# Performance work log

Measured on AMD Instinct MI355X. Metric: run time of the kernel, lower is better.

## Reference

```python
import math
import jax, jax.numpy as jnp
import numpy as np

B, T, E, H = 8, 2048, 512, 8
NQ_H, NL = 4, 2          # qubits per attention head, circuit layers
NQ_F, FFN = 8, 2048      # FFN qubits, ffn_dim

# ---- batched state-vector quantum simulation -------------------------------
# state shape: [N, 2, 2, ..., 2] (one axis of size 2 per qubit; wire q = axis q+1)

def apply_ry(state, q, theta):
    """RY(theta) on wire q. theta: scalar or [N] (per-batch angle)."""
    th = jnp.asarray(theta) * 0.5
    c, s = jnp.cos(th), jnp.sin(th)
    if th.ndim == 1:
        shp = (-1,) + (1,) * (state.ndim - 2)
        c, s = c.reshape(shp), s.reshape(shp)
    s0 = jax.lax.index_in_dim(state, 0, axis=q + 1, keepdims=False)
    s1 = jax.lax.index_in_dim(state, 1, axis=q + 1, keepdims=False)
    return jnp.stack([c * s0 - s * s1, s * s0 + c * s1], axis=q + 1)

def apply_cnot(state, ctrl, tgt):
    c0 = jax.lax.index_in_dim(state, 0, axis=ctrl + 1, keepdims=True)
    c1 = jax.lax.index_in_dim(state, 1, axis=ctrl + 1, keepdims=True)
    c1 = jnp.flip(c1, axis=tgt + 1)  # X on target when control = 1
    return jnp.concatenate([c0, c1], axis=ctrl + 1)

def run_circuit(x, params):
    """x: [N, n] data angles. params: [L, n] (shared) or [N, L, n] (per-element).
    Circuit: L x (RY(params) layer + CNOT chain + ring CNOT), then RY(x), then <Z_q>.
    Returns [N, n] PauliZ expectations."""
    N, n = x.shape
    L = params.shape[-2]
    state = jnp.zeros((N, 2 ** n), x.dtype).at[:, 0].set(1.0).reshape((N,) + (2,) * n)
    for l in range(L):
        for q in range(n):
            theta = params[:, l, q] if params.ndim == 3 else params[l, q]
            state = apply_ry(state, q, theta)
        for q in range(n - 1):
            state = apply_cnot(state, q, q + 1)
        state = apply_cnot(state, n - 1, 0)
    for q in range(n):
        state = apply_ry(state, q, x[:, q])
    probs = (state ** 2).reshape(N, 2 ** n)
    bits = (jnp.arange(2 ** n)[:, None] >> (n - 1 - jnp.arange(n))) & 1  # wire 0 = MSB
    return probs @ (1 - 2 * bits).astype(x.dtype)  # [N, n]

def layer_norm(x, g, b, eps=1e-5):
    m = x.mean(-1, keepdims=True)
    v = ((x - m) ** 2).mean(-1, keepdims=True)
    return (x - m) / jnp.sqrt(v + eps) * g + b

def setup_inputs() -> dict:
    key = jax.random.key(0)
    ks = jax.random.split(key, 9)
    def lin(k, o, i):
        return jax.random.normal(k, (o, i), jnp.float32) / np.sqrt(i).astype(np.float32)
    return {
        "x": jax.random.normal(ks[0], (B, T, E), jnp.float32),
        "wq": lin(ks[1], E, E), "wk": lin(ks[2], E, E),
        "wv": lin(ks[3], E, E), "wo": lin(ks[4], E, E),
        "head_params": jax.random.normal(ks[5], (H, NL, NQ_H), jnp.float32),
        "ffn_params": jax.random.normal(ks[6], (2, NQ_F), jnp.float32),
        "w1": lin(ks[7], FFN, NQ_F), "w2": lin(ks[8], E, FFN),
        "g1": jnp.ones((E,), jnp.float32), "b1": jnp.zeros((E,), jnp.float32),
        "g2": jnp.ones((E,), jnp.float32), "b2": jnp.zeros((E,), jnp.float32),
    }

def reference(x, wq, wk, wv, wo, head_params, ffn_params, w1, w2, g1, b1, g2, b2):
    Bb, Tt, Ee = x.shape
    hd = Ee // H
    BT = Bb * Tt
    # ---- quantum multi-head attention (dropout = eval/identity) ----
    q = x @ wq.T; k = x @ wk.T; v = x @ wv.T
    scores = jnp.einsum('bte,bse->bts', q, k) / math.sqrt(Ee)  # NOTE: scale by sqrt(E)
    attn = jax.nn.softmax(scores, axis=-1)
    out = jnp.einsum('bts,bse->bte', attn, v)                  # [B,T,E]
    oh = out.reshape(Bb, Tt, H, hd)
    # fold heads into the batch dim; per-head params broadcast per element
    xh = oh[..., :NQ_H].transpose(2, 0, 1, 3).reshape(H * BT, NQ_H)
    ph = jnp.broadcast_to(head_params[:, None], (H, BT, NL, NQ_H)).reshape(H * BT, NL, NQ_H)
    qout = run_circuit(xh, ph)                                  # [H*BT, NQ_H]
    qout = jnp.pad(qout, ((0, 0), (0, hd - NQ_H)))              # zero-pad to head_dim
    qout = qout.reshape(H, Bb, Tt, hd).transpose(1, 2, 0, 3).reshape(Bb, Tt, Ee)
    attn_out = qout @ wo.T
    x1 = layer_norm(x + attn_out, g1, b1)
    # ---- quantum FFN (only ffn_params[0] used, as in source) ----
    xf = x1.reshape(BT, Ee)[:, :NQ_F]
    f = run_circuit(xf, ffn_params[:1]).reshape(Bb, Tt, NQ_F)
    f = jax.nn.relu(f @ w1.T) @ w2.T
    return layer_norm(x1 + f, g2, b2)
```

## Files before the change

kernel.cpp:

```cpp
#include <hip/hip_runtime.h>
#include <hip/hip_bf16.h>
#include <math.h>


#define B_   8
#define T_   2048
#define E_   512

typedef __attribute__((ext_vector_type(8))) short bf16x8;
typedef __attribute__((ext_vector_type(4))) short bf16x4;
typedef __attribute__((ext_vector_type(4))) float f32x4;

#define GLL16(g, l) __builtin_amdgcn_global_load_lds((const __attribute__((address_space(1))) void*)(g), (__attribute__((address_space(3))) void*)(l), 16, 0, 0)

__device__ inline unsigned short f2bf(float f){
  union { float f; unsigned u; } v; v.f = f;
  unsigned r = v.u + 0x7fff + ((v.u >> 16) & 1);
  return (unsigned short)(r >> 16);
}

__global__ __launch_bounds__(256) void k0_setup(const float* __restrict__ hp,
                         const float* __restrict__ fp,
                         const float* __restrict__ wo, float* __restrict__ cAB,
                         unsigned short* __restrict__ wo32b) {
  int t = threadIdx.x, bi = blockIdx.x;
  if (bi > 0) {
    int gid = (bi-1)*256 + t;
    int e = gid >> 3, c4 = gid & 7;
    float4 v = *(const float4*)(wo + (size_t)e*512 + c4*64);
    unsigned short h[4] = { f2bf(v.x), f2bf(v.y), f2bf(v.z), f2bf(v.w) };
    *(unsigned long long*)(wo32b + (size_t)e*32 + c4*4) = *(unsigned long long*)h;
    return;
  }
  __shared__ float fst[256], tmp[256], ra[256], rb[256];
  fst[t] = (t == 0) ? 1.f : 0.f;
  __syncthreads();
  #pragma unroll
  for (int q = 0; q < 8; ++q) {
    int str = 1 << (7-q);
    float th = 0.5f * fp[q];
    float c = cosf(th), s = sinf(th);
    float self = fst[t], part = fst[t ^ str];
    float nv = (t & str) ? (c*self + s*part) : (c*self - s*part);
    __syncthreads();
    tmp[t] = nv;
    __syncthreads();
    fst[t] = tmp[t];
    __syncthreads();
  }
  #pragma unroll
  for (int g = 0; g < 8; ++g) {
    int ctrl = (g < 7) ? g : 7, tgt = (g < 7) ? g+1 : 0;
    int cs = 1 << (7-ctrl), tsr = 1 << (7-tgt);
    float nv = fst[(t & cs) ? (t ^ tsr) : t];
    __syncthreads();
    fst[t] = nv;
    __syncthreads();
  }
  #pragma unroll
  for (int q = 0; q < 8; ++q) {
    int str = 1 << (7-q);
    float a = fst[t]*fst[t] * ((t & str) ? -1.f : 1.f);
    float b = fst[t]*fst[t ^ str];
    ra[t] = a; rb[t] = b;
    __syncthreads();
    for (int off = 128; off > 0; off >>= 1){
      if (t < off){ ra[t] += ra[t+off]; rb[t] += rb[t+off]; }
      __syncthreads();
    }
    if (t == 0){ cAB[64+q] = ra[0]; cAB[72+q] = rb[0]; }
    __syncthreads();
  }
  if (t < 8) {
    float st[16];
    #pragma unroll
    for (int i=0;i<16;i++) st[i]=0.f;
    st[0]=1.f;
    for (int l=0;l<2;l++){
      for (int q=0;q<4;q++){
        float th = 0.5f*hp[t*8 + l*4 + q];
        float c = cosf(th), s = sinf(th);
        int str = 1<<(3-q);
        for (int i=0;i<16;i++) if (!(i & str)) {
          float s0=st[i], s1=st[i|str];
          st[i]     = c*s0 - s*s1;
          st[i|str] = s*s0 + c*s1;
        }
      }
      for (int q=0;q<4;q++){
        int ctrl = (q<3)? q : 3, tgt = (q<3)? q+1 : 0;
        int cs = 1<<(3-ctrl), tsr = 1<<(3-tgt);
        for (int i=0;i<16;i++) if ((i&cs) && !(i&tsr)) {
          float tt = st[i]; st[i]=st[i|tsr]; st[i|tsr]=tt;
        }
      }
    }
    for (int q=0;q<4;q++){
      int str = 1<<(3-q);
      float A=0.f, Bv=0.f;
      for (int i=0;i<16;i++){
        A  += st[i]*st[i] * ((i&str)? -1.f : 1.f);
        Bv += st[i]*st[i^str];
      }
      cAB[t*4+q]    = A;
      cAB[32+t*4+q] = Bv;
    }
  }
}

__global__ __launch_bounds__(256) void kc_cast(const float* __restrict__ x,
                     const float* __restrict__ wq, const float* __restrict__ wk,
                     const float* __restrict__ w2, const float* __restrict__ wv,
                     unsigned short* __restrict__ xb, unsigned short* __restrict__ wqkb,
                     unsigned short* __restrict__ w2b, unsigned short* __restrict__ wv32b){
  int bi = blockIdx.x;
  if (bi < 4096) {
    int i = bi*256 + threadIdx.x;
    const float4* p = (const float4*)x + (size_t)i*2;
    float4 a = p[0], b = p[1];
    union { unsigned short h[8]; uint4 u; } o;
    o.h[0]=f2bf(a.x); o.h[1]=f2bf(a.y); o.h[2]=f2bf(a.z); o.h[3]=f2bf(a.w);
    o.h[4]=f2bf(b.x); o.h[5]=f2bf(b.y); o.h[6]=f2bf(b.z); o.h[7]=f2bf(b.w);
    ((uint4*)xb)[i] = o.u;
    return;
  }
  int i = (bi-4096)*256 + threadIdx.x;
  const float* src; unsigned short* dst; float s = 1.f;
  if (i < 65536){
    int row = i >> 6, c8 = (i & 63)*8;
    if (row < 512){ src = wq + (size_t)row*512 + c8; s = 0.044194173824159216f; }
    else          { src = wk + (size_t)(row-512)*512 + c8; }
    dst = wqkb + (size_t)row*512 + c8;
  } else if (i < 196608){
    int j = i - 65536;
    src = w2 + (size_t)j*8; dst = w2b + (size_t)j*8;
  } else {
    int j = i - 196608;
    int r = j >> 6, c8 = (j & 63)*8;
    src = wv + (size_t)((r>>2)*64 + (r&3))*512 + c8;
    dst = wv32b + (size_t)r*512 + c8;
  }
  float4 a = *(const float4*)src, b = *(const float4*)(src+4);
  union { unsigned short h[8]; uint4 u; } o;
  o.h[0]=f2bf(a.x*s); o.h[1]=f2bf(a.y*s); o.h[2]=f2bf(a.z*s); o.h[3]=f2bf(a.w*s);
  o.h[4]=f2bf(b.x*s); o.h[5]=f2bf(b.y*s); o.h[6]=f2bf(b.z*s); o.h[7]=f2bf(b.w*s);
  *(uint4*)dst = o.u;
}

template<int K, int LDC, bool OUTBF, int GX, int GM>
__global__ __launch_bounds__(256,2) void gemm_bt(
    const unsigned short* __restrict__ A, const unsigned short* __restrict__ Bw,
    void* __restrict__ C, int m_base){
  __shared__ __align__(16) char sm[16384];
  char* As = sm; char* Bs = sm + 8192;
  int t = threadIdx.x, w = t>>6, l = t&63;
  int lr = l&15, quad = l>>4;
  int lin = blockIdx.x;
  int n0 = ((lin >> 3) % GX) * 128;
  int m0 = ((lin & 7) * (GM/8) + lin / (8*GX)) * 128;
  int wr = (w>>1)*64, wc = (w&1)*64;
  f32x4 acc[4][4] = {};
  for (int k0 = 0; k0 < K; k0 += 32){
    __syncthreads();
    #pragma unroll
    for (int c = 0; c < 2; ++c){
      int ch = c*256 + t, row = ch>>2, sw = ch&3, lc = sw ^ ((row>>1)&3);
      GLL16(A  + (size_t)(m0+row)*K + k0 + lc*8, As + c*4096 + w*1024);
      GLL16(Bw + (size_t)(n0+row)*K + k0 + lc*8, Bs + c*4096 + w*1024);
    }
    __syncthreads();
    bf16x8 af[4], bg[4];
    #pragma unroll
    for (int i=0;i<4;++i){
      int ra = wr + i*16 + lr;
      af[i] = *(const bf16x8*)(As + ra*64 + (quad ^ ((ra>>1)&3))*16);
      int rb = wc + i*16 + lr;
      bg[i] = *(const bf16x8*)(Bs + rb*64 + (quad ^ ((rb>>1)&3))*16);
    }
    #pragma unroll
    for (int i=0;i<4;++i)
      #pragma unroll
      for (int j=0;j<4;++j)
        acc[i][j] = __builtin_amdgcn_mfma_f32_16x16x32_bf16(af[i], bg[j], acc[i][j], 0,0,0);
  }
  #pragma unroll
  for (int i=0;i<4;++i)
    #pragma unroll
    for (int j=0;j<4;++j)
      #pragma unroll
      for (int r=0;r<4;++r){
        size_t row = (size_t)(m_base + m0 + wr + i*16 + quad*4 + r);
        int col = n0 + wc + j*16 + lr;
        if constexpr (OUTBF) ((unsigned short*)C)[row*LDC + col] = f2bf(acc[i][j][r]);
        else                 ((float*)C)[row*LDC + col] = acc[i][j][r];
      }
}

__global__ __launch_bounds__(256) void k1_v32m(const unsigned short* __restrict__ xb,
    const unsigned short* __restrict__ wv32b, unsigned short* __restrict__ v32t){
  __shared__ __align__(16) char sm1[98304];
  char* Xs = sm1; char* Ws = sm1 + 65536;
  int t = threadIdx.x, w = t>>6, l = t&63, lr = l&15, quad = l>>4;
  int m0 = blockIdx.x * 64;
  #pragma unroll
  for (int i=0;i<16;++i){
    int p = i*256 + t, ks = p>>8, c2 = p&255, row = c2>>2, swp = c2&3;
    int lc = swp ^ ((row>>1)&3);
    GLL16(xb + (size_t)(m0+row)*512 + ks*32 + lc*8, Xs + (p>>6)*1024);
  }
  #pragma unroll
  for (int i=0;i<8;++i){
    int p = i*256 + t, ks = p>>7, c2 = p&127, row = c2>>2, swp = c2&3;
    int lc = swp ^ ((row>>1)&3);
    GLL16(wv32b + (size_t)row*512 + ks*32 + lc*8, Ws + (p>>6)*1024);
  }
  __syncthreads();
  f32x4 acc[2] = {};
  #pragma unroll
  for (int ks=0; ks<16; ++ks){
    int xrow = w*16 + lr;
    bf16x8 bq = *(const bf16x8*)(Xs + ks*4096 + xrow*64 + (quad ^ ((xrow>>1)&3))*16);
    #pragma unroll
    for (int ni=0; ni<2; ++ni){
      int wrow = ni*16 + lr;
      bf16x8 af = *(const bf16x8*)(Ws + ks*2048 + wrow*64 + (quad ^ ((wrow>>1)&3))*16);
      acc[ni] = __builtin_amdgcn_mfma_f32_16x16x32_bf16(af, bq, acc[ni], 0,0,0);
    }
  }
  int bb = m0 >> 11, sbase = (m0 & 2047) + w*16 + lr;
  #pragma unroll
  for (int ni=0; ni<2; ++ni)
    #pragma unroll
    for (int r=0; r<4; ++r){
      int c = ni*16 + quad*4 + r;
      v32t[((size_t)(bb*32 + c))*2048 + sbase] = f2bf(acc[ni][r]);
    }
}

__global__ __launch_bounds__(256,2) void k2_attn(
    const unsigned short* __restrict__ qkb, const unsigned short* __restrict__ v32t,
    float* __restrict__ Opart, float* __restrict__ mlb){
  __shared__ __align__(16) char sm[77824];
  char* Qc  = sm;
  char* Ks  = sm + 16384;
  char* Vts = sm + 49152;
  float* OtL = (float*)sm;
  float* mL  = (float*)(sm + 73728);
  float* lL  = (float*)(sm + 75776);

  int t = threadIdx.x, w = t>>6, l = t&63;
  int lr = l & 15, quad = l >> 4;
  int lin = blockIdx.x;
  int b = lin & 7;
  int m0 = ((lin >> 3) & 15) * 128;
  int half = lin >> 7;
  size_t bT = (size_t)b*2048;
  const char* qbase = (const char*)qkb + (bT + m0)*2048;
  const char* vbase = (const char*)v32t + (size_t)b*32*4096;

  f32x4 Ot[2][8] = {};
  float mold[8], lsum[8];
  #pragma unroll
  for (int qj=0;qj<8;++qj){ mold[qj] = -1e30f; lsum[qj] = 0.f; }

  for (int st = 0; st < 2; ++st){
    int s0 = (half*2 + st)*256;
    const char* kbase = (const char*)qkb + (bT + s0)*2048 + 1024;
    __syncthreads();
    {
      int j = t>>3, seg = t&7;
      const uint4* vs = (const uint4*)(vbase + (size_t)j*4096 + (s0 + seg*32)*2);
      uint4* vd = (uint4*)(Vts + j*528 + seg*64);
      vd[0]=vs[0]; vd[1]=vs[1]; vd[2]=vs[2]; vd[3]=vs[3];
    }
    f32x4 acc[4][8] = {};
    for (int ec = 0; ec < 8; ++ec){
      __syncthreads();
      #pragma unroll
      for (int u = 0; u < 4; ++u){
        int kk = u>>1, c = u&1;
        int ch = c*256 + t, row = ch>>2, sw = ch&3, lc = sw ^ ((row>>1)&3);
        GLL16(qbase + (size_t)row*2048 + ec*128 + kk*64 + lc*16,
              Qc + kk*8192 + c*4096 + w*1024);
      }
      #pragma unroll
      for (int rd = 0; rd < 4; ++rd){
        int ch = rd*256 + t, row = ch>>2, sw = ch&3, lc = sw ^ ((row>>1)&3);
        GLL16(kbase + (size_t)row*2048 + ec*128 +      lc*16, Ks +         rd*4096 + w*1024);
        GLL16(kbase + (size_t)row*2048 + ec*128 + 64 + lc*16, Ks + 16384 + rd*4096 + w*1024);
      }
      __syncthreads();
      #pragma unroll
      for (int kk = 0; kk < 2; ++kk){
        bf16x8 af[4];
        #pragma unroll
        for (int si = 0; si < 4; ++si){
          int row = w*64 + si*16 + lr;
          af[si] = *(const bf16x8*)(Ks + kk*16384 + row*64 + (quad ^ ((row>>1)&3))*16);
        }
        #pragma unroll
        for (int qh = 0; qh < 2; ++qh){
          bf16x8 bq[4];
          #pragma unroll
          for (int jj = 0; jj < 4; ++jj){
            int row = (qh*4+jj)*16 + lr;
            bq[jj] = *(const bf16x8*)(Qc + kk*8192 + row*64 + (quad ^ ((row>>1)&3))*16);
          }
          __builtin_amdgcn_s_setprio(1);
          #pragma unroll
          for (int si = 0; si < 4; ++si)
            #pragma unroll
            for (int jj = 0; jj < 4; ++jj)
              acc[si][qh*4+jj] = __builtin_amdgcn_mfma_f32_16x16x32_bf16(af[si], bq[jj], acc[si][qh*4+jj], 0,0,0);
          __builtin_amdgcn_s_setprio(0);
        }
      }
    }
    bf16x4 aV[2][4];
    #pragma unroll
    for (int vt=0; vt<2; ++vt)
      #pragma unroll
      for (int si=0; si<4; ++si)
        aV[vt][si] = *(const bf16x4*)(Vts + (vt*16+lr)*528 + (w*64 + si*16 + quad*4)*2);
    #pragma unroll
    for (int qj=0; qj<8; ++qj){
      float mt = -1e30f;
      #pragma unroll
      for (int si=0; si<4; ++si)
        #pragma unroll
        for (int r=0;r<4;++r) mt = fmaxf(mt, acc[si][qj][r]);
      mt = fmaxf(mt, __shfl_xor(mt, 16));
      mt = fmaxf(mt, __shfl_xor(mt, 32));
      float mn = fmaxf(mold[qj], mt);
      float al = __expf(mold[qj] - mn);
      mold[qj] = mn;
      float rs = 0.f;
      #pragma unroll
      for (int si=0; si<4; ++si)
        #pragma unroll
        for (int r=0;r<4;++r){
          float p = __expf(acc[si][qj][r] - mn);
          acc[si][qj][r] = p; rs += p;
        }
      rs += __shfl_xor(rs, 16); rs += __shfl_xor(rs, 32);
      lsum[qj] = lsum[qj]*al + rs;
      Ot[0][qj] *= al; Ot[1][qj] *= al;
      #pragma unroll
      for (int si=0; si<4; ++si){
        bf16x4 pb;
        pb[0]=(short)f2bf(acc[si][qj][0]); pb[1]=(short)f2bf(acc[si][qj][1]);
        pb[2]=(short)f2bf(acc[si][qj][2]); pb[3]=(short)f2bf(acc[si][qj][3]);
        Ot[0][qj] = __builtin_amdgcn_mfma_f32_16x16x16bf16_1k(aV[0][si], pb, Ot[0][qj], 0,0,0);
        Ot[1][qj] = __builtin_amdgcn_mfma_f32_16x16x16bf16_1k(aV[1][si], pb, Ot[1][qj], 0,0,0);
      }
    }
  }
  __syncthreads();
  #pragma unroll
  for (int qj=0; qj<8; ++qj){
    if (quad == 0){ mL[w*128 + qj*16 + lr] = mold[qj]; lL[w*128 + qj*16 + lr] = lsum[qj]; }
    *(f32x4*)(OtL + (size_t)(w*128 + qj*16 + lr)*36 + quad*4)      = Ot[0][qj];
    *(f32x4*)(OtL + (size_t)(w*128 + qj*16 + lr)*36 + 16 + quad*4) = Ot[1][qj];
  }
  __syncthreads();
  #pragma unroll
  for (int u=0; u<2; ++u){
    int qr = u*64 + (t>>2), vg = (t&3)*8;
    float M = -1e30f;
    #pragma unroll
    for (int w4=0; w4<4; ++w4) M = fmaxf(M, mL[w4*128+qr]);
    float L = 0.f; float o[8] = {};
    #pragma unroll
    for (int w4=0; w4<4; ++w4){
      float a = __expf(mL[w4*128+qr] - M);
      L += a * lL[w4*128+qr];
      const float* Op = OtL + (size_t)(w4*128+qr)*36 + vg;
      #pragma unroll
      for (int j=0;j<8;++j) o[j] += a*Op[j];
    }
    size_t tok = bT + m0 + qr;
    float* od = Opart + ((size_t)half*16384 + tok)*32 + vg;
    *(float4*)od     = make_float4(o[0],o[1],o[2],o[3]);
    *(float4*)(od+4) = make_float4(o[4],o[5],o[6],o[7]);
    if ((t&3) == 0){
      mlb[((size_t)half*16384 + tok)*2]     = M;
      mlb[((size_t)half*16384 + tok)*2 + 1] = L;
    }
  }
}

__global__ __launch_bounds__(256) void k3_proj_ln(const float* __restrict__ x,
    const float* __restrict__ Opart, const float* __restrict__ mlb,
    const unsigned short* __restrict__ wo32b,
    const float* __restrict__ g1, const float* __restrict__ b1,
    const float* __restrict__ cAB, float* __restrict__ x1, float* __restrict__ fbuf) {
  __shared__ __align__(16) char sm3[36224];
  char* Ws = sm3;
  char* Qs = sm3 + 32768;
  float* red1 = (float*)(sm3 + 34816);
  float* red2 = (float*)(sm3 + 35328);
  float* mm   = (float*)(sm3 + 35840);
  float* rr   = (float*)(sm3 + 35968);
  int t = threadIdx.x, w = t>>6, l = t&63, lr = l&15, quad = l>>4;
  int tok0 = blockIdx.x * 32;
  #pragma unroll
  for (int i=0;i<8;++i){
    int g = t + i*256, row = g>>2, ch = g&3;
    uint4 v = ((const uint4*)wo32b)[g];
    *(uint4*)(Ws + row*64 + (ch ^ ((row>>1)&3))*16) = v;
  }
  {
    int tokL = t>>3, cg = t&7;
    size_t gt = (size_t)tok0 + tokL;
    float m[4], lv[4];
    #pragma unroll
    for (int h=0;h<4;++h){
      m[h]  = mlb[((size_t)h*16384 + gt)*2];
      lv[h] = mlb[((size_t)h*16384 + gt)*2 + 1];
    }
    float M = fmaxf(fmaxf(m[0],m[1]), fmaxf(m[2],m[3]));
    float a[4], L = 0.f;
    #pragma unroll
    for (int h=0;h<4;++h){ a[h] = __expf(m[h]-M); L += a[h]*lv[h]; }
    float inv = 1.f / L;
    float o[4] = {};
    #pragma unroll
    for (int h=0;h<4;++h){
      float4 v = *(const float4*)(Opart + ((size_t)h*16384 + gt)*32 + cg*4);
      o[0] += a[h]*v.x; o[1] += a[h]*v.y; o[2] += a[h]*v.z; o[3] += a[h]*v.w;
    }
    bf16x4 qv;
    #pragma unroll
    for (int j=0;j<4;++j){
      float ov = o[j] * inv;
      int cc = cg*4 + j;
      qv[j] = (short)f2bf(cosf(ov)*cAB[cc] - sinf(ov)*cAB[32+cc]);
    }
    *(bf16x4*)(Qs + tokL*64 + (((cg>>1) ^ ((tokL>>1)&3))<<4) + ((cg&1)<<3)) = qv;
  }
  __syncthreads();
  bf16x8 af[2], bf[8];
  #pragma unroll
  for (int i=0;i<2;++i){
    int m = i*16 + lr;
    af[i] = *(const bf16x8*)(Qs + m*64 + (quad ^ ((m>>1)&3))*16);
  }
  #pragma unroll
  for (int j=0;j<8;++j){
    int n = w*128 + j*16 + lr;
    bf[j] = *(const bf16x8*)(Ws + n*64 + (quad ^ ((n>>1)&3))*16);
  }
  f32x4 acc[2][8];
  #pragma unroll
  for (int i=0;i<2;++i)
    #pragma unroll
    for (int j=0;j<8;++j){
      f32x4 z = {0.f,0.f,0.f,0.f};
      acc[i][j] = __builtin_amdgcn_mfma_f32_16x16x32_bf16(af[i], bf[j], z, 0,0,0);
    }
  float s1[2][4] = {}, s2[2][4] = {};
  #pragma unroll
  for (int i=0;i<2;++i)
    #pragma unroll
    for (int r=0;r<4;++r){
      int m = i*16 + quad*4 + r;
      const float* xrow = x + (size_t)(tok0+m)*512 + w*128 + lr;
      #pragma unroll
      for (int j=0;j<8;++j){
        float v = acc[i][j][r] + xrow[j*16];
        acc[i][j][r] = v;
        s1[i][r] += v; s2[i][r] += v*v;
      }
    }
  #pragma unroll
  for (int off=1; off<16; off<<=1){
    #pragma unroll
    for (int i=0;i<2;++i)
      #pragma unroll
      for (int r=0;r<4;++r){
        s1[i][r] += __shfl_xor(s1[i][r], off);
        s2[i][r] += __shfl_xor(s2[i][r], off);
      }
  }
  if (lr == 0){
    #pragma unroll
    for (int i=0;i<2;++i)
      #pragma unroll
      for (int r=0;r<4;++r){
        int m = i*16 + quad*4 + r;
        red1[w*32 + m] = s1[i][r];
        red2[w*32 + m] = s2[i][r];
      }
  }
  __syncthreads();
  if (t < 32){
    float a = red1[t] + red1[32+t] + red1[64+t] + red1[96+t];
    float bb = red2[t] + red2[32+t] + red2[64+t] + red2[96+t];
    float mean = a * (1.f/512.f);
    float var  = bb * (1.f/512.f) - mean*mean;
    mm[t] = mean; rr[t] = rsqrtf(var + 1e-5f);
  }
  __syncthreads();
  float g1v[8], b1v[8];
  #pragma unroll
  for (int j=0;j<8;++j){
    int n = w*128 + j*16 + lr;
    g1v[j] = g1[n]; b1v[j] = b1[n];
  }
  #pragma unroll
  for (int i=0;i<2;++i)
    #pragma unroll
    for (int r=0;r<4;++r){
      int m = i*16 + quad*4 + r;
      float mean = mm[m], rstd = rr[m];
      float* orow = x1 + (size_t)(tok0+m)*512 + w*128 + lr;
      #pragma unroll
      for (int j=0;j<8;++j){
        float nv = (acc[i][j][r]-mean)*rstd*g1v[j] + b1v[j];
        orow[j*16] = nv;
        if (w == 0 && j == 0 && lr < 8)
          fbuf[(size_t)(tok0+m)*8 + lr] = cosf(nv)*cAB[64+lr] - sinf(nv)*cAB[72+lr];
      }
    }
}

__global__ __launch_bounds__(256) void k4a4(const float* __restrict__ fbuf,
    const float* __restrict__ w1, unsigned short* __restrict__ Hb, int row0){
  __shared__ float w1s[16384];
  int t = threadIdx.x;
  #pragma unroll
  for (int i=0;i<16;++i){
    int p = i*256 + t;
    *(float4*)(w1s + (size_t)p*4) = *(const float4*)(w1 + (size_t)p*4);
  }
  __syncthreads();
  float wv[8][8];
  #pragma unroll
  for (int i=0;i<16;++i){
    float4 v = *(const float4*)(w1s + t*64 + i*4);
    wv[i>>1][(i&1)*4+0]=v.x; wv[i>>1][(i&1)*4+1]=v.y;
    wv[i>>1][(i&1)*4+2]=v.z; wv[i>>1][(i&1)*4+3]=v.w;
  }
  int tokL = blockIdx.x * 32;
  #pragma unroll 2
  for (int u=0;u<32;++u){
    const float4* fp4 = (const float4*)(fbuf + (size_t)(row0 + tokL + u)*8);
    float4 fa = fp4[0], fb = fp4[1];
    union { unsigned short h[8]; uint4 q; } o;
    #pragma unroll
    for (int j=0;j<8;++j){
      float s = fa.x*wv[j][0] + fa.y*wv[j][1] + fa.z*wv[j][2] + fa.w*wv[j][3]
              + fb.x*wv[j][4] + fb.y*wv[j][5] + fb.z*wv[j][6] + fb.w*wv[j][7];
      o.h[j] = f2bf(fmaxf(s, 0.f));
    }
    *(uint4*)(Hb + (size_t)(tokL + u)*2048 + t*8) = o.q;
  }
}

__global__ __launch_bounds__(256) void k5_ln2(const float* __restrict__ x1,
    const float* __restrict__ g2, const float* __restrict__ b2,
    float* __restrict__ out) {
  int tok = blockIdx.x, t = threadIdx.x;
  __shared__ float rs1[4], rs2[4], mv[2];
  float vals[2], ssum=0.f, ssq=0.f;
  #pragma unroll
  for (int u=0;u<2;u++){
    int e = t + u*256;
    float s = x1[(size_t)tok*512 + e] + out[(size_t)tok*512 + e];
    vals[u]=s; ssum+=s; ssq+=s*s;
  }
  #pragma unroll
  for (int off=32; off>0; off>>=1){ ssum += __shfl_down(ssum,off); ssq += __shfl_down(ssq,off); }
  int wid = t >> 6;
  if ((t & 63) == 0){ rs1[wid]=ssum; rs2[wid]=ssq; }
  __syncthreads();
  if (t == 0){
    float a = rs1[0]+rs1[1]+rs1[2]+rs1[3];
    float b = rs2[0]+rs2[1]+rs2[2]+rs2[3];
    float mean = a * (1.f/512.f);
    float var  = b * (1.f/512.f) - mean*mean;
    mv[0]=mean; mv[1]=rsqrtf(var + 1e-5f);
  }
  __syncthreads();
  float mean=mv[0], rstd=mv[1];
  #pragma unroll
  for (int u=0;u<2;u++){
    int e = t + u*256;
    out[(size_t)tok*512 + e] = (vals[u]-mean)*rstd*g2[e] + b2[e];
  }
}

extern "C" void kernel_launch(void* const* d_in, const int* in_sizes, int n_in,
                              void* d_out, int out_size, void* d_ws, size_t ws_size,
                              hipStream_t stream) {
  const float* x  = (const float*)d_in[0];
  const float* wq = (const float*)d_in[1];
  const float* wk = (const float*)d_in[2];
  const float* wv = (const float*)d_in[3];
  const float* wo = (const float*)d_in[4];
  const float* hp = (const float*)d_in[5];
  const float* fp = (const float*)d_in[6];
  const float* w1 = (const float*)d_in[7];
  const float* w2 = (const float*)d_in[8];
  const float* g1 = (const float*)d_in[9];
  const float* b1 = (const float*)d_in[10];
  const float* g2 = (const float*)d_in[11];
  const float* b2 = (const float*)d_in[12];
  float* out = (float*)d_out;
  float* ws  = (float*)d_ws;

  unsigned short* qkb  = (unsigned short*)(ws);
  float*          x1   = ws + 8388608;
  unsigned short* xb   = (unsigned short*)(ws + 16777216);
  unsigned short* wqkb = (unsigned short*)(ws + 20971520);
  unsigned short* w2b  = (unsigned short*)(ws + 21233664);
  unsigned short* v32t = (unsigned short*)(ws + 21757952);
  float*          fbuf = ws + 22544384;
  unsigned short* wo32b= (unsigned short*)(ws + 22675456);
  float*          cAB  = ws + 22691840;
  float*          mlb  = ws + 22691968;
  unsigned short* wv32b= (unsigned short*)(ws + 23806080);
  float*          Opart= ws + 16777216;
  unsigned short* Hb   = (unsigned short*)(ws);

  k0_setup<<<17, 256, 0, stream>>>(hp, fp, wo, cAB, wo32b);
  kc_cast<<<4872, 256, 0, stream>>>(x, wq, wk, w2, wv, xb, wqkb, w2b, wv32b);
  gemm_bt<512,1024,true,8,128><<<1024, 256, 0, stream>>>(xb, wqkb, qkb, 0);
  k1_v32m<<<256, 256, 0, stream>>>(xb, wv32b, v32t);
  k2_attn<<<512, 256, 0, stream>>>(qkb, v32t, Opart, mlb);
  k3_proj_ln<<<512, 256, 0, stream>>>(x, Opart, mlb, wo32b, g1, b1, cAB, x1, fbuf);
  k4a4<<<256, 256, 0, stream>>>(fbuf, w1, Hb, 0);
  gemm_bt<2048,512,false,4,64><<<256, 256, 0, stream>>>(Hb, w2b, out, 0);
  k4a4<<<256, 256, 0, stream>>>(fbuf, w1, Hb, 8192);
  gemm_bt<2048,512,false,4,64><<<256, 256, 0, stream>>>(Hb, w2b, out, 8192);
  k5_ln2<<<16384, 256, 0, stream>>>(x1, g2, b2, out);
}
```

Before: 373.8 us.

## Fold Wq^T Wk into a single matrix so scores use x directly as keys

Precomputes M = (Wk^T Wq) scaled by 1/sqrt(E) with a small transpose-and-GEMM step, then projects only x·M into a query buffer and uses bf16 x directly as the key operand in attention. This halves the QK projection GEMM and its output traffic, and shrinks the per-row stride read by the attention kernel. It adds a transpose kernel and a tiny GEMM, and rounding the folded product to bf16 slightly changes numerics. Separately, the final layernorm is rewritten to handle one token per wavefront with vectorized loads and shuffle-only reductions, removing shared-memory syncs.

```diff
diff --git a/kernel.cpp b/kernel.cpp
--- a/kernel.cpp
+++ b/kernel.cpp
@@ -109,10 +109,9 @@
 }
 
 __global__ __launch_bounds__(256) void kc_cast(const float* __restrict__ x,
-                     const float* __restrict__ wq, const float* __restrict__ wk,
                      const float* __restrict__ w2, const float* __restrict__ wv,
-                     unsigned short* __restrict__ xb, unsigned short* __restrict__ wqkb,
-                     unsigned short* __restrict__ w2b, unsigned short* __restrict__ wv32b){
+                     unsigned short* __restrict__ xb, unsigned short* __restrict__ w2b,
+                     unsigned short* __restrict__ wv32b){
   int bi = blockIdx.x;
   if (bi < 4096) {
     int i = bi*256 + threadIdx.x;
@@ -125,26 +124,88 @@
     return;
   }
   int i = (bi-4096)*256 + threadIdx.x;
-  const float* src; unsigned short* dst; float s = 1.f;
-  if (i < 65536){
-    int row = i >> 6, c8 = (i & 63)*8;
-    if (row < 512){ src = wq + (size_t)row*512 + c8; s = 0.044194173824159216f; }
-    else          { src = wk + (size_t)(row-512)*512 + c8; }
-    dst = wqkb + (size_t)row*512 + c8;
-  } else if (i < 196608){
-    int j = i - 65536;
-    src = w2 + (size_t)j*8; dst = w2b + (size_t)j*8;
+  const float* src; unsigned short* dst;
+  if (i < 131072){
+    src = w2 + (size_t)i*8; dst = w2b + (size_t)i*8;
   } else {
-    int j = i - 196608;
+    int j = i - 131072;
     int r = j >> 6, c8 = (j & 63)*8;
     src = wv + (size_t)((r>>2)*64 + (r&3))*512 + c8;
     dst = wv32b + (size_t)r*512 + c8;
   }
   float4 a = *(const float4*)src, b = *(const float4*)(src+4);
   union { unsigned short h[8]; uint4 u; } o;
-  o.h[0]=f2bf(a.x*s); o.h[1]=f2bf(a.y*s); o.h[2]=f2bf(a.z*s); o.h[3]=f2bf(a.w*s);
-  o.h[4]=f2bf(b.x*s); o.h[5]=f2bf(b.y*s); o.h[6]=f2bf(b.z*s); o.h[7]=f2bf(b.w*s);
+  o.h[0]=f2bf(a.x); o.h[1]=f2bf(a.y); o.h[2]=f2bf(a.z); o.h[3]=f2bf(a.w);
+  o.h[4]=f2bf(b.x); o.h[5]=f2bf(b.y); o.h[6]=f2bf(b.z); o.h[7]=f2bf(b.w);
   *(uint4*)dst = o.u;
+}
+
+__global__ __launch_bounds__(256) void ktr(const float* __restrict__ wq,
+    const float* __restrict__ wk, unsigned short* __restrict__ wqT,
+    unsigned short* __restrict__ wkT){
+  __shared__ float ts[64][65];
+  int bi = blockIdx.x, t = threadIdx.x;
+  const float* src = (bi & 1) ? wk : wq;
+  unsigned short* dst = (bi & 1) ? wkT : wqT;
+  int tile = bi >> 1;
+  int r0 = (tile >> 3) * 64, c0 = (tile & 7) * 64;
+  int row = t >> 2, cb = (t & 3) * 16;
+  #pragma unroll
+  for (int u=0; u<4; ++u)
+    *(float4*)&ts[row][cb + u*4] = *(const float4*)(src + (size_t)(r0+row)*512 + c0 + cb + u*4);
+  __syncthreads();
+  unsigned short h[16];
+  #pragma unroll
+  for (int k=0;k<16;++k) h[k] = f2bf(ts[cb + k][row]);
+  *(uint4*)(dst + (size_t)(c0+row)*512 + r0 + cb)     = *(uint4*)h;
+  *(uint4*)(dst + (size_t)(c0+row)*512 + r0 + cb + 8) = *(uint4*)(h+8);
+}
+
+__global__ __launch_bounds__(256,2) void gemm_mm(
+    const unsigned short* __restrict__ A, const unsigned short* __restrict__ Bw,
+    unsigned short* __restrict__ C){
+  __shared__ __align__(16) char sm[16384];
+  char* As = sm; char* Bs = sm + 8192;
+  int t = threadIdx.x, w = t>>6, l = t&63;
+  int lr = l&15, quad = l>>4;
+  int lin = blockIdx.x;
+  int n0 = (lin & 3) * 128;
+  int m0 = (lin >> 2) * 128;
+  int wr = (w>>1)*64, wc = (w&1)*64;
+  f32x4 acc[4][4] = {};
+  for (int k0 = 0; k0 < 512; k0 += 32){
+    __syncthreads();
+    #pragma unroll
+    for (int c = 0; c < 2; ++c){
+      int ch = c*256 + t, row = ch>>2, sw = ch&3, lc = sw ^ ((row>>1)&3);
+      GLL16(A  + (size_t)(m0+row)*512 + k0 + lc*8, As + c*4096 + w*1024);
+      GLL16(Bw + (size_t)(n0+row)*512 + k0 + lc*8, Bs + c*4096 + w*1024);
+    }
+    __syncthreads();
+    bf16x8 af[4], bg[4];
+    #pragma unroll
+    for (int i=0;i<4;++i){
+      int ra = wr + i*16 + lr;
+      af[i] = *(const bf16x8*)(As + ra*64 + (quad ^ ((ra>>1)&3))*16);
+      int rb = wc + i*16 + lr;
+      bg[i] = *(const bf16x8*)(Bs + rb*64 + (quad ^ ((rb>>1)&3))*16);
+    }
+    #pragma unroll
+    for (int i=0;i<4;++i)
+      #pragma unroll
+      for (int j=0;j<4;++j)
+        acc[i][j] = __builtin_amdgcn_mfma_f32_16x16x32_bf16(af[i], bg[j], acc[i][j], 0,0,0);
+  }
+  #pragma unroll
+  for (int i=0;i<4;++i)
+    #pragma unroll
+    for (int j=0;j<4;++j)
+      #pragma unroll
+      for (int r=0;r<4;++r){
+        size_t row = (size_t)(m0 + wr + i*16 + quad*4 + r);
+        int col = n0 + wc + j*16 + lr;
+        C[row*512 + col] = f2bf(acc[i][j][r] * 0.044194173824159216f);
+      }
 }
 
 template<int K, int LDC, bool OUTBF, int GX, int GM>
@@ -238,7 +299,8 @@
 }
 
 __global__ __launch_bounds__(256,2) void k2_attn(
-    const unsigned short* __restrict__ qkb, const unsigned short* __restrict__ v32t,
+    const unsigned short* __restrict__ qb, const unsigned short* __restrict__ kb,
+    const unsigned short* __restrict__ v32t,
     float* __restrict__ Opart, float* __restrict__ mlb){
   __shared__ __align__(16) char sm[77824];
   char* Qc  = sm;
@@ -255,7 +317,7 @@
   int m0 = ((lin >> 3) & 15) * 128;
   int half = lin >> 7;
   size_t bT = (size_t)b*2048;
-  const char* qbase = (const char*)qkb + (bT + m0)*2048;
+  const char* qbase = (const char*)qb + (bT + m0)*1024;
   const char* vbase = (const char*)v32t + (size_t)b*32*4096;
 
   f32x4 Ot[2][8] = {};
@@ -265,7 +327,7 @@
 
   for (int st = 0; st < 2; ++st){
     int s0 = (half*2 + st)*256;
-    const char* kbase = (const char*)qkb + (bT + s0)*2048 + 1024;
+    const char* kbase = (const char*)kb + (bT + s0)*1024;
     __syncthreads();
     {
       int j = t>>3, seg = t&7;
@@ -280,14 +342,14 @@
       for (int u = 0; u < 4; ++u){
         int kk = u>>1, c = u&1;
         int ch = c*256 + t, row = ch>>2, sw = ch&3, lc = sw ^ ((row>>1)&3);
-        GLL16(qbase + (size_t)row*2048 + ec*128 + kk*64 + lc*16,
+        GLL16(qbase + (size_t)row*1024 + ec*128 + kk*64 + lc*16,
               Qc + kk*8192 + c*4096 + w*1024);
       }
       #pragma unroll
       for (int rd = 0; rd < 4; ++rd){
         int ch = rd*256 + t, row = ch>>2, sw = ch&3, lc = sw ^ ((row>>1)&3);
-        GLL16(kbase + (size_t)row*2048 + ec*128 +      lc*16, Ks +         rd*4096 + w*1024);
-        GLL16(kbase + (size_t)row*2048 + ec*128 + 64 + lc*16, Ks + 16384 + rd*4096 + w*1024);
+        GLL16(kbase + (size_t)row*1024 + ec*128 +      lc*16, Ks +         rd*4096 + w*1024);
+        GLL16(kbase + (size_t)row*1024 + ec*128 + 64 + lc*16, Ks + 16384 + rd*4096 + w*1024);
       }
       __syncthreads();
       #pragma unroll
@@ -560,34 +622,34 @@
 __global__ __launch_bounds__(256) void k5_ln2(const float* __restrict__ x1,
     const float* __restrict__ g2, const float* __restrict__ b2,
     float* __restrict__ out) {
-  int tok = blockIdx.x, t = threadIdx.x;
-  __shared__ float rs1[4], rs2[4], mv[2];
-  float vals[2], ssum=0.f, ssq=0.f;
-  #pragma unroll
-  for (int u=0;u<2;u++){
-    int e = t + u*256;
-    float s = x1[(size_t)tok*512 + e] + out[(size_t)tok*512 + e];
-    vals[u]=s; ssum+=s; ssq+=s*s;
-  }
-  #pragma unroll
-  for (int off=32; off>0; off>>=1){ ssum += __shfl_down(ssum,off); ssq += __shfl_down(ssq,off); }
-  int wid = t >> 6;
-  if ((t & 63) == 0){ rs1[wid]=ssum; rs2[wid]=ssq; }
-  __syncthreads();
-  if (t == 0){
-    float a = rs1[0]+rs1[1]+rs1[2]+rs1[3];
-    float b = rs2[0]+rs2[1]+rs2[2]+rs2[3];
-    float mean = a * (1.f/512.f);
-    float var  = b * (1.f/512.f) - mean*mean;
-    mv[0]=mean; mv[1]=rsqrtf(var + 1e-5f);
-  }
-  __syncthreads();
-  float mean=mv[0], rstd=mv[1];
-  #pragma unroll
-  for (int u=0;u<2;u++){
-    int e = t + u*256;
-    out[(size_t)tok*512 + e] = (vals[u]-mean)*rstd*g2[e] + b2[e];
-  }
+  int t = threadIdx.x, w = t>>6, lane = t&63;
+  size_t tok = (size_t)blockIdx.x*4 + w;
+  const float* xr = x1 + tok*512 + lane*8;
+  float* orow = out + tok*512 + lane*8;
+  float4 a = *(const float4*)xr, b = *(const float4*)(xr+4);
+  float4 oa = *(const float4*)orow, ob = *(const float4*)(orow+4);
+  float v[8] = {a.x+oa.x, a.y+oa.y, a.z+oa.z, a.w+oa.w,
+                b.x+ob.x, b.y+ob.y, b.z+ob.z, b.w+ob.w};
+  float ssum=0.f, ssq=0.f;
+  #pragma unroll
+  for (int j=0;j<8;++j){ ssum += v[j]; ssq += v[j]*v[j]; }
+  #pragma unroll
+  for (int off=1; off<64; off<<=1){
+    ssum += __shfl_xor(ssum, off);
+    ssq  += __shfl_xor(ssq, off);
+  }
+  float mean = ssum * (1.f/512.f);
+  float var  = ssq * (1.f/512.f) - mean*mean;
+  float rstd = rsqrtf(var + 1e-5f);
+  float4 ga = *(const float4*)(g2 + lane*8), gb = *(const float4*)(g2 + lane*8 + 4);
+  float4 ba = *(const float4*)(b2 + lane*8), bb = *(const float4*)(b2 + lane*8 + 4);
+  float g[8] = {ga.x,ga.y,ga.z,ga.w, gb.x,gb.y,gb.z,gb.w};
+  float bi[8] = {ba.x,ba.y,ba.z,ba.w, bb.x,bb.y,bb.z,bb.w};
+  float o[8];
+  #pragma unroll
+  for (int j=0;j<8;++j) o[j] = (v[j]-mean)*rstd*g[j] + bi[j];
+  *(float4*)orow     = make_float4(o[0],o[1],o[2],o[3]);
+  *(float4*)(orow+4) = make_float4(o[4],o[5],o[6],o[7]);
 }
 
 extern "C" void kernel_launch(void* const* d_in, const int* in_sizes, int n_in,
@@ -609,29 +671,33 @@
   float* out = (float*)d_out;
   float* ws  = (float*)d_ws;
 
-  unsigned short* qkb  = (unsigned short*)(ws);
+  unsigned short* qb   = (unsigned short*)(ws);
+  unsigned short* xb   = (unsigned short*)(ws + 4194304);
   float*          x1   = ws + 8388608;
-  unsigned short* xb   = (unsigned short*)(ws + 16777216);
-  unsigned short* wqkb = (unsigned short*)(ws + 20971520);
-  unsigned short* w2b  = (unsigned short*)(ws + 21233664);
-  unsigned short* v32t = (unsigned short*)(ws + 21757952);
-  float*          fbuf = ws + 22544384;
-  unsigned short* wo32b= (unsigned short*)(ws + 22675456);
-  float*          cAB  = ws + 22691840;
-  float*          mlb  = ws + 22691968;
-  unsigned short* wv32b= (unsigned short*)(ws + 23806080);
-  float*          Opart= ws + 16777216;
+  unsigned short* w2b  = (unsigned short*)(ws + 16777216);
+  unsigned short* v32t = (unsigned short*)(ws + 17301504);
+  float*          fbuf = ws + 17825792;
+  unsigned short* wo32b= (unsigned short*)(ws + 17956864);
+  float*          cAB  = ws + 17965056;
+  float*          mlb  = ws + 17965184;
+  unsigned short* wv32b= (unsigned short*)(ws + 18096256);
+  unsigned short* wqTb = (unsigned short*)(ws + 18104448);
+  unsigned short* wkTb = (unsigned short*)(ws + 18235520);
+  unsigned short* Mb   = (unsigned short*)(ws + 18366592);
+  float*          Opart= ws + 18497664;
   unsigned short* Hb   = (unsigned short*)(ws);
 
   k0_setup<<<17, 256, 0, stream>>>(hp, fp, wo, cAB, wo32b);
-  kc_cast<<<4872, 256, 0, stream>>>(x, wq, wk, w2, wv, xb, wqkb, w2b, wv32b);
-  gemm_bt<512,1024,true,8,128><<<1024, 256, 0, stream>>>(xb, wqkb, qkb, 0);
+  kc_cast<<<4616, 256, 0, stream>>>(x, w2, wv, xb, w2b, wv32b);
+  ktr<<<128, 256, 0, stream>>>(wq, wk, wqTb, wkTb);
+  gemm_mm<<<16, 256, 0, stream>>>(wkTb, wqTb, Mb);
+  gemm_bt<512,512,true,4,128><<<512, 256, 0, stream>>>(xb, Mb, qb, 0);
   k1_v32m<<<256, 256, 0, stream>>>(xb, wv32b, v32t);
-  k2_attn<<<512, 256, 0, stream>>>(qkb, v32t, Opart, mlb);
+  k2_attn<<<512, 256, 0, stream>>>(qb, xb, v32t, Opart, mlb);
   k3_proj_ln<<<512, 256, 0, stream>>>(x, Opart, mlb, wo32b, g1, b1, cAB, x1, fbuf);
   k4a4<<<256, 256, 0, stream>>>(fbuf, w1, Hb, 0);
   gemm_bt<2048,512,false,4,64><<<256, 256, 0, stream>>>(Hb, w2b, out, 0);
   k4a4<<<256, 256, 0, stream>>>(fbuf, w1, Hb, 8192);
   gemm_bt<2048,512,false,4,64><<<256, 256, 0, stream>>>(Hb, w2b, out, 8192);
-  k5_ln2<<<16384, 256, 0, stream>>>(x1, g2, b2, out);
-}
+  k5_ln2<<<4096, 256, 0, stream>>>(x1, g2, b2, out);
+}
```

After: 374.5 us. No clear change (+0.2%).
